# Optimization experiments

Measured on AMD Instinct MI355X. Metric: run time of the kernel, lower is better.

Reference implementation:

```python
import jax, jax.numpy as jnp
import numpy as np

NTOKENS = 50257
NHID = 1024
NPC = int(np.ceil(np.sqrt(NTOKENS)))            # 225 tokens per class
NCLASSES = int(np.ceil(NTOKENS / NPC))          # 224 classes
BATCH = 1024
INITRANGE = 0.1


def setup_inputs() -> dict:
    key = jax.random.key(0)
    k1, k2, k3, k4 = jax.random.split(key, 4)
    inputs = jax.random.normal(k1, (BATCH, NHID), dtype=jnp.float32)
    labels = jax.random.randint(k2, (BATCH,), 0, NTOKENS, dtype=jnp.int64)
    layer_top_W = jax.random.uniform(k3, (NHID, NCLASSES), minval=-INITRANGE, maxval=INITRANGE, dtype=jnp.float32)
    layer_top_b = jnp.zeros((NCLASSES,), dtype=jnp.float32)
    layer_bottom_W = jax.random.uniform(k4, (NCLASSES, NHID, NPC), minval=-INITRANGE, maxval=INITRANGE, dtype=jnp.float32)
    layer_bottom_b = jnp.zeros((NCLASSES, NPC), dtype=jnp.float32)
    return {
        "inputs": inputs,
        "labels": labels,
        "layer_top_W": layer_top_W,
        "layer_top_b": layer_top_b,
        "layer_bottom_W": layer_bottom_W,
        "layer_bottom_b": layer_bottom_b,
    }


def reference(inputs, labels, layer_top_W, layer_top_b, layer_bottom_W, layer_bottom_b):
    batch_size = inputs.shape[0]
    # decompose label into (class, within-class) position; old-torch `/` on Long == floor div
    pos_top = labels // NPC            # [B]
    pos_bottom = labels % NPC          # [B]

    # top-level class distribution: [B, nclasses]
    top_logits = inputs @ layer_top_W + layer_top_b
    top_probs = jax.nn.softmax(top_logits, axis=1)

    # gather per-sample class weight slices and do batched matvec:
    # layer_bottom_W[pos_top]: [B, nhid, npc]
    bottom_logits = jnp.einsum("bd,bdc->bc", inputs, layer_bottom_W[pos_top]) + layer_bottom_b[pos_top]
    bottom_probs = jax.nn.softmax(bottom_logits, axis=1)

    rows = jnp.arange(batch_size)
    target_probs = top_probs[rows, pos_top] * bottom_probs[rows, pos_bottom]  # [B]
    return target_probs
```

## Files before the change

### kernel.cpp

```cpp
#include <hip/hip_runtime.h>
#include <math.h>

#define NHID 1024
#define NPC  225
#define NCLS 224
#define BATCH 1024
#define N_TOP (BATCH / 8)

#define WS_PT 0
#define WS_PB 1024

__global__ __launch_bounds__(1024, 4) void k_fused(const float* __restrict__ X,
                                                   const int* __restrict__ labels,
                                                   const float* __restrict__ Wt,
                                                   const float* __restrict__ bt,
                                                   const float* __restrict__ Wb,
                                                   const float* __restrict__ bb,
                                                   float* __restrict__ ws)
{
    __shared__ __align__(16) float sm[14848];
    __shared__ int slist[128];
    __shared__ int scnt;

    const int tid  = threadIdx.x;
    const int wave = tid >> 6;
    const int lane = tid & 63;
    const int j8   = tid & 7;
    const int t8   = tid >> 3;

    if ((int)blockIdx.x < NCLS) {
        const int cls = blockIdx.x;
        if (tid == 0) scnt = 0;
        __syncthreads();
        {
            const int lab = labels[tid];
            if (lab / NPC == cls) {
                const int p = atomicAdd(&scnt, 1);
                if (p < 128) slist[p] = tid;
            }
        }
        __syncthreads();
        const int cnt = scnt;
        if (cnt == 0) return;

        const int c0 = lane, c1 = lane + 64, c2 = lane + 128, c3 = lane + 192;
        const bool m3 = (c3 < NPC);
        const int d0 = wave * 64;
        const float* Wr = Wb + (size_t)cls * (NHID * NPC) + (size_t)d0 * NPC;

        for (int base = 0; base < cnt; base += 8) {
            const int nt = min(8, cnt - base);

            const int sid = (j8 < nt) ? slist[base + j8] : -1;
            for (int d4 = t8; d4 < 256; d4 += 128) {
                float4 v = make_float4(0.f, 0.f, 0.f, 0.f);
                if (sid >= 0) v = ((const float4*)&X[(size_t)sid * NHID])[d4];
                float* p = &sm[48 * d4 + j8];
                p[0] = v.x; p[12] = v.y; p[24] = v.z; p[36] = v.w;
            }
            __syncthreads();

            float acc[8][4];
#pragma unroll
            for (int j = 0; j < 8; ++j)
#pragma unroll
                for (int k = 0; k < 4; ++k) acc[j][k] = 0.f;

            auto ldrow = [&](int r, float* o) {
                const float* p = Wr + (size_t)r * NPC;
                o[0] = __builtin_nontemporal_load(p + c0);
                o[1] = __builtin_nontemporal_load(p + c1);
                o[2] = __builtin_nontemporal_load(p + c2);
                o[3] = m3 ? __builtin_nontemporal_load(p + c3) : 0.f;
            };
            float wbuf[4][4];
            ldrow(0, wbuf[0]); ldrow(1, wbuf[1]); ldrow(2, wbuf[2]); ldrow(3, wbuf[3]);

#pragma unroll 4
            for (int dd = 0; dd < 64; ++dd) {
                const int slot = dd & 3;
                const float cw0 = wbuf[slot][0], cw1 = wbuf[slot][1],
                            cw2 = wbuf[slot][2], cw3 = wbuf[slot][3];
                ldrow(min(dd + 4, 63), wbuf[slot]);
                const float4 a = *(const float4*)&sm[(d0 + dd) * 12 + 0];
                const float4 b = *(const float4*)&sm[(d0 + dd) * 12 + 4];
                const float xi[8] = {a.x, a.y, a.z, a.w, b.x, b.y, b.z, b.w};
#pragma unroll
                for (int j = 0; j < 8; ++j) {
                    acc[j][0] = fmaf(xi[j], cw0, acc[j][0]);
                    acc[j][1] = fmaf(xi[j], cw1, acc[j][1]);
                    acc[j][2] = fmaf(xi[j], cw2, acc[j][2]);
                    acc[j][3] = fmaf(xi[j], cw3, acc[j][3]);
                }
            }
            __syncthreads();

            float* red = sm;
            if (wave >= 8) {
#pragma unroll
                for (int j = 0; j < 8; ++j)
#pragma unroll
                    for (int k = 0; k < 4; ++k) {
                        int c = lane + 64 * k;
                        if (c < NPC) red[((wave - 8) * 8 + j) * 232 + c] = acc[j][k];
                    }
            }
            __syncthreads();
            if (wave < 8) {
#pragma unroll
                for (int j = 0; j < 8; ++j)
#pragma unroll
                    for (int k = 0; k < 4; ++k) {
                        int c = lane + 64 * k;
                        if (c < NPC) red[(wave * 8 + j) * 232 + c] += acc[j][k];
                    }
            }
            __syncthreads();

            if (wave < 8) {
                const int j = wave;
                if (j < nt) {
                    const int s = slist[base + j];
                    float v[4];
#pragma unroll
                    for (int k = 0; k < 4; ++k) {
                        int c = lane + 64 * k;
                        if (c < NPC) {
                            float t = bb[(size_t)cls * NPC + c];
#pragma unroll
                            for (int g = 0; g < 8; ++g) t += red[(g * 8 + j) * 232 + c];
                            v[k] = t;
                        } else v[k] = -INFINITY;
                    }
                    float m = fmaxf(fmaxf(v[0], v[1]), fmaxf(v[2], v[3]));
                    for (int o = 32; o > 0; o >>= 1) m = fmaxf(m, __shfl_xor(m, o));
                    float e = expf(v[0] - m) + expf(v[1] - m) + expf(v[2] - m) + expf(v[3] - m);
                    for (int o = 32; o > 0; o >>= 1) e += __shfl_xor(e, o);
                    const int pb = labels[s] % NPC;
                    if (lane == (pb & 63))
                        ws[WS_PB + s] = expf(v[pb >> 6] - m) / e;
                }
            }
            __syncthreads();
        }
        return;
    }

    const int sbase = (blockIdx.x - NCLS) * 8;

    for (int d4 = t8; d4 < 256; d4 += 128) {
        const float4 v = ((const float4*)&X[(size_t)(sbase + j8) * NHID])[d4];
        float* p = &sm[48 * d4 + j8];
        p[0] = v.x; p[12] = v.y; p[24] = v.z; p[36] = v.w;
    }
    __syncthreads();

    float acc[8][4];
#pragma unroll
    for (int j = 0; j < 8; ++j)
#pragma unroll
        for (int k = 0; k < 4; ++k) acc[j][k] = 0.f;

    const int c0 = lane, c1 = lane + 64, c2 = lane + 128, c3 = lane + 192;
    const bool m3 = (c3 < NCLS);
    const int d0 = wave * 64;
    const float* Wr = Wt + (size_t)d0 * NCLS;

    auto ldrow = [&](int r, float* o) {
        const float* p = Wr + (size_t)r * NCLS;
        o[0] = p[c0]; o[1] = p[c1]; o[2] = p[c2];
        o[3] = m3 ? p[c3] : 0.f;
    };
    float wbuf[4][4];
    ldrow(0, wbuf[0]); ldrow(1, wbuf[1]); ldrow(2, wbuf[2]); ldrow(3, wbuf[3]);

#pragma unroll 4
    for (int dd = 0; dd < 64; ++dd) {
        const int slot = dd & 3;
        const float cw0 = wbuf[slot][0], cw1 = wbuf[slot][1],
                    cw2 = wbuf[slot][2], cw3 = wbuf[slot][3];
        ldrow(min(dd + 4, 63), wbuf[slot]);
        const float4 a = *(const float4*)&sm[(d0 + dd) * 12 + 0];
        const float4 b = *(const float4*)&sm[(d0 + dd) * 12 + 4];
        const float xi[8] = {a.x, a.y, a.z, a.w, b.x, b.y, b.z, b.w};
#pragma unroll
        for (int j = 0; j < 8; ++j) {
            acc[j][0] = fmaf(xi[j], cw0, acc[j][0]);
            acc[j][1] = fmaf(xi[j], cw1, acc[j][1]);
            acc[j][2] = fmaf(xi[j], cw2, acc[j][2]);
            acc[j][3] = fmaf(xi[j], cw3, acc[j][3]);
        }
    }
    __syncthreads();

    float* red = sm;
    if (wave >= 8) {
#pragma unroll
        for (int j = 0; j < 8; ++j)
#pragma unroll
            for (int k = 0; k < 4; ++k) {
                int c = lane + 64 * k;
                if (c < NCLS) red[((wave - 8) * 8 + j) * 232 + c] = acc[j][k];
            }
    }
    __syncthreads();
    if (wave < 8) {
#pragma unroll
        for (int j = 0; j < 8; ++j)
#pragma unroll
            for (int k = 0; k < 4; ++k) {
                int c = lane + 64 * k;
                if (c < NCLS) red[(wave * 8 + j) * 232 + c] += acc[j][k];
            }
    }
    __syncthreads();

    if (wave < 8) {
        const int j = wave;
        const int s = sbase + j;
        float v[4];
#pragma unroll
        for (int k = 0; k < 4; ++k) {
            int c = lane + 64 * k;
            if (c < NCLS) {
                float t = bt[c];
#pragma unroll
                for (int g = 0; g < 8; ++g) t += red[(g * 8 + j) * 232 + c];
                v[k] = t;
            } else v[k] = -INFINITY;
        }
        float m = fmaxf(fmaxf(v[0], v[1]), fmaxf(v[2], v[3]));
        for (int o = 32; o > 0; o >>= 1) m = fmaxf(m, __shfl_xor(m, o));
        float e = expf(v[0] - m) + expf(v[1] - m) + expf(v[2] - m) + expf(v[3] - m);
        for (int o = 32; o > 0; o >>= 1) e += __shfl_xor(e, o);
        const int pt = labels[s] / NPC;
        if (lane == (pt & 63))
            ws[WS_PT + s] = expf(v[pt >> 6] - m) / e;
    }
}

__global__ void k_mul(const float* __restrict__ ws, float* __restrict__ out)
{
    const int i = blockIdx.x * 256 + threadIdx.x;
    if (i < BATCH) out[i] = ws[WS_PT + i] * ws[WS_PB + i];
}

extern "C" void kernel_launch(void* const* d_in, const int* in_sizes, int n_in,
                              void* d_out, int out_size, void* d_ws, size_t ws_size,
                              hipStream_t stream)
{
    const float* X      = (const float*)d_in[0];
    const int*   labels = (const int*)  d_in[1];
    const float* Wt     = (const float*)d_in[2];
    const float* bt     = (const float*)d_in[3];
    const float* Wb     = (const float*)d_in[4];
    const float* bb     = (const float*)d_in[5];

    hipLaunchKernelGGL(k_fused, dim3(NCLS + N_TOP), dim3(1024), 0, stream,
                       X, labels, Wt, bt, Wb, bb, (float*)d_ws);
    hipLaunchKernelGGL(k_mul, dim3(BATCH / 256), dim3(256), 0, stream,
                       (const float*)d_ws, (float*)d_out);
}
```

Measured before the change: 345.8 us.

## Split bottom-layer work into one block per 8-sample chunk of each class

```diff
diff --git a/kernel.cpp b/kernel.cpp
--- a/kernel.cpp
+++ b/kernel.cpp
@@ -5,6 +5,7 @@
 #define NPC  225
 #define NCLS 224
 #define BATCH 1024
+#define N_BOT 352
 #define N_TOP (BATCH / 8)
 
 #define WS_PT 0
@@ -19,8 +20,11 @@
                                                    float* __restrict__ ws)
 {
     __shared__ __align__(16) float sm[14848];
-    __shared__ int slist[128];
-    __shared__ int scnt;
+    __shared__ int cnt_[256];
+    __shared__ int iscan_[256];
+    __shared__ int slot[8];
+    __shared__ int wtot[16];
+    __shared__ int cls_sh;
 
     const int tid  = threadIdx.x;
     const int wave = tid >> 6;
@@ -28,125 +32,148 @@
     const int j8   = tid & 7;
     const int t8   = tid >> 3;
 
-    if ((int)blockIdx.x < NCLS) {
-        const int cls = blockIdx.x;
-        if (tid == 0) scnt = 0;
-        __syncthreads();
+    if ((int)blockIdx.x < N_BOT) {
+        if (tid < 256) cnt_[tid] = 0;
+        __syncthreads();
+        const int myc = labels[tid] / NPC;
+        atomicAdd(&cnt_[myc], 1);
+        __syncthreads();
+        if (tid < 256) iscan_[tid] = (tid < NCLS) ? ((cnt_[tid] + 7) >> 3) : 0;
+        __syncthreads();
+        for (int off = 1; off < 256; off <<= 1) {
+            int a = 0;
+            if (tid < 256 && tid >= off) a = iscan_[tid - off];
+            __syncthreads();
+            if (tid < 256) iscan_[tid] += a;
+            __syncthreads();
+        }
+        if ((int)blockIdx.x >= iscan_[255]) return;
+        if (tid < NCLS) {
+            const int lo = (tid == 0) ? 0 : iscan_[tid - 1];
+            if ((int)blockIdx.x >= lo && (int)blockIdx.x < iscan_[tid]) cls_sh = tid;
+        }
+        __syncthreads();
+        const int cls    = cls_sh;
+        const int ibase  = (cls == 0) ? 0 : iscan_[cls - 1];
+        const int within = (int)blockIdx.x - ibase;
+        const int cnt    = cnt_[cls];
+        const int nt     = min(8, cnt - 8 * within);
+
         {
-            const int lab = labels[tid];
-            if (lab / NPC == cls) {
-                const int p = atomicAdd(&scnt, 1);
-                if (p < 128) slist[p] = tid;
-            }
-        }
-        __syncthreads();
-        const int cnt = scnt;
-        if (cnt == 0) return;
+            const bool flag = (myc == cls);
+            const unsigned long long m = __ballot(flag);
+            if (lane == 0) wtot[wave] = __popcll(m);
+            __syncthreads();
+            if (flag) {
+                int pos = __popcll(m & ((1ull << lane) - 1));
+#pragma unroll
+                for (int w = 0; w < 16; ++w)
+                    if (w < wave) pos += wtot[w];
+                const int r = pos - 8 * within;
+                if (r >= 0 && r < 8) slot[r] = tid;
+            }
+            __syncthreads();
+        }
+
+        const int sid = (j8 < nt) ? slot[j8] : -1;
+        for (int d4 = t8; d4 < 256; d4 += 128) {
+            float4 v = make_float4(0.f, 0.f, 0.f, 0.f);
+            if (sid >= 0) v = ((const float4*)&X[(size_t)sid * NHID])[d4];
+            float* p = &sm[48 * d4 + j8];
+            p[0] = v.x; p[12] = v.y; p[24] = v.z; p[36] = v.w;
+        }
+        __syncthreads();
+
+        float acc[8][4];
+#pragma unroll
+        for (int j = 0; j < 8; ++j)
+#pragma unroll
+            for (int k = 0; k < 4; ++k) acc[j][k] = 0.f;
 
         const int c0 = lane, c1 = lane + 64, c2 = lane + 128, c3 = lane + 192;
         const bool m3 = (c3 < NPC);
         const int d0 = wave * 64;
         const float* Wr = Wb + (size_t)cls * (NHID * NPC) + (size_t)d0 * NPC;
 
-        for (int base = 0; base < cnt; base += 8) {
-            const int nt = min(8, cnt - base);
-
-            const int sid = (j8 < nt) ? slist[base + j8] : -1;
-            for (int d4 = t8; d4 < 256; d4 += 128) {
-                float4 v = make_float4(0.f, 0.f, 0.f, 0.f);
-                if (sid >= 0) v = ((const float4*)&X[(size_t)sid * NHID])[d4];
-                float* p = &sm[48 * d4 + j8];
-                p[0] = v.x; p[12] = v.y; p[24] = v.z; p[36] = v.w;
-            }
-            __syncthreads();
-
-            float acc[8][4];
+        auto ldrow = [&](int r, float* o) {
+            const float* p = Wr + (size_t)r * NPC;
+            o[0] = __builtin_nontemporal_load(p + c0);
+            o[1] = __builtin_nontemporal_load(p + c1);
+            o[2] = __builtin_nontemporal_load(p + c2);
+            o[3] = m3 ? __builtin_nontemporal_load(p + c3) : 0.f;
+        };
+        float wbuf[4][4];
+        ldrow(0, wbuf[0]); ldrow(1, wbuf[1]); ldrow(2, wbuf[2]); ldrow(3, wbuf[3]);
+
+#pragma unroll 4
+        for (int dd = 0; dd < 64; ++dd) {
+            const int slot4 = dd & 3;
+            const float cw0 = wbuf[slot4][0], cw1 = wbuf[slot4][1],
+                        cw2 = wbuf[slot4][2], cw3 = wbuf[slot4][3];
+            ldrow(min(dd + 4, 63), wbuf[slot4]);
+            const float4 a = *(const float4*)&sm[(d0 + dd) * 12 + 0];
+            const float4 b = *(const float4*)&sm[(d0 + dd) * 12 + 4];
+            const float xi[8] = {a.x, a.y, a.z, a.w, b.x, b.y, b.z, b.w};
+#pragma unroll
+            for (int j = 0; j < 8; ++j) {
+                acc[j][0] = fmaf(xi[j], cw0, acc[j][0]);
+                acc[j][1] = fmaf(xi[j], cw1, acc[j][1]);
+                acc[j][2] = fmaf(xi[j], cw2, acc[j][2]);
+                acc[j][3] = fmaf(xi[j], cw3, acc[j][3]);
+            }
+        }
+        __syncthreads();
+
+        float* red = sm;
+        if (wave >= 8) {
 #pragma unroll
             for (int j = 0; j < 8; ++j)
 #pragma unroll
-                for (int k = 0; k < 4; ++k) acc[j][k] = 0.f;
-
-            auto ldrow = [&](int r, float* o) {
-                const float* p = Wr + (size_t)r * NPC;
-                o[0] = __builtin_nontemporal_load(p + c0);
-                o[1] = __builtin_nontemporal_load(p + c1);
-                o[2] = __builtin_nontemporal_load(p + c2);
-                o[3] = m3 ? __builtin_nontemporal_load(p + c3) : 0.f;
-            };
-            float wbuf[4][4];
-            ldrow(0, wbuf[0]); ldrow(1, wbuf[1]); ldrow(2, wbuf[2]); ldrow(3, wbuf[3]);
-
-#pragma unroll 4
-            for (int dd = 0; dd < 64; ++dd) {
-                const int slot = dd & 3;
-                const float cw0 = wbuf[slot][0], cw1 = wbuf[slot][1],
-                            cw2 = wbuf[slot][2], cw3 = wbuf[slot][3];
-                ldrow(min(dd + 4, 63), wbuf[slot]);
-                const float4 a = *(const float4*)&sm[(d0 + dd) * 12 + 0];
-                const float4 b = *(const float4*)&sm[(d0 + dd) * 12 + 4];
-                const float xi[8] = {a.x, a.y, a.z, a.w, b.x, b.y, b.z, b.w};
-#pragma unroll
-                for (int j = 0; j < 8; ++j) {
-                    acc[j][0] = fmaf(xi[j], cw0, acc[j][0]);
-                    acc[j][1] = fmaf(xi[j], cw1, acc[j][1]);
-                    acc[j][2] = fmaf(xi[j], cw2, acc[j][2]);
-                    acc[j][3] = fmaf(xi[j], cw3, acc[j][3]);
+                for (int k = 0; k < 4; ++k) {
+                    int c = lane + 64 * k;
+                    if (c < NPC) red[((wave - 8) * 8 + j) * 232 + c] = acc[j][k];
                 }
-            }
-            __syncthreads();
-
-            float* red = sm;
-            if (wave >= 8) {
-#pragma unroll
-                for (int j = 0; j < 8; ++j)
-#pragma unroll
-                    for (int k = 0; k < 4; ++k) {
-                        int c = lane + 64 * k;
-                        if (c < NPC) red[((wave - 8) * 8 + j) * 232 + c] = acc[j][k];
-                    }
-            }
-            __syncthreads();
-            if (wave < 8) {
-#pragma unroll
-                for (int j = 0; j < 8; ++j)
-#pragma unroll
-                    for (int k = 0; k < 4; ++k) {
-                        int c = lane + 64 * k;
-                        if (c < NPC) red[(wave * 8 + j) * 232 + c] += acc[j][k];
-                    }
-            }
-            __syncthreads();
-
-            if (wave < 8) {
-                const int j = wave;
-                if (j < nt) {
-                    const int s = slist[base + j];
-                    float v[4];
-#pragma unroll
-                    for (int k = 0; k < 4; ++k) {
-                        int c = lane + 64 * k;
-                        if (c < NPC) {
-                            float t = bb[(size_t)cls * NPC + c];
-#pragma unroll
-                            for (int g = 0; g < 8; ++g) t += red[(g * 8 + j) * 232 + c];
-                            v[k] = t;
-                        } else v[k] = -INFINITY;
-                    }
-                    float m = fmaxf(fmaxf(v[0], v[1]), fmaxf(v[2], v[3]));
-                    for (int o = 32; o > 0; o >>= 1) m = fmaxf(m, __shfl_xor(m, o));
-                    float e = expf(v[0] - m) + expf(v[1] - m) + expf(v[2] - m) + expf(v[3] - m);
-                    for (int o = 32; o > 0; o >>= 1) e += __shfl_xor(e, o);
-                    const int pb = labels[s] % NPC;
-                    if (lane == (pb & 63))
-                        ws[WS_PB + s] = expf(v[pb >> 6] - m) / e;
+        }
+        __syncthreads();
+        if (wave < 8) {
+#pragma unroll
+            for (int j = 0; j < 8; ++j)
+#pragma unroll
+                for (int k = 0; k < 4; ++k) {
+                    int c = lane + 64 * k;
+                    if (c < NPC) red[(wave * 8 + j) * 232 + c] += acc[j][k];
                 }
-            }
-            __syncthreads();
+        }
+        __syncthreads();
+
+        if (wave < 8) {
+            const int j = wave;
+            if (j < nt) {
+                const int s = slot[j];
+                float v[4];
+#pragma unroll
+                for (int k = 0; k < 4; ++k) {
+                    int c = lane + 64 * k;
+                    if (c < NPC) {
+                        float t = bb[(size_t)cls * NPC + c];
+#pragma unroll
+                        for (int g = 0; g < 8; ++g) t += red[(g * 8 + j) * 232 + c];
+                        v[k] = t;
+                    } else v[k] = -INFINITY;
+                }
+                float m = fmaxf(fmaxf(v[0], v[1]), fmaxf(v[2], v[3]));
+                for (int o = 32; o > 0; o >>= 1) m = fmaxf(m, __shfl_xor(m, o));
+                float e = expf(v[0] - m) + expf(v[1] - m) + expf(v[2] - m) + expf(v[3] - m);
+                for (int o = 32; o > 0; o >>= 1) e += __shfl_xor(e, o);
+                const int pb = labels[s] % NPC;
+                if (lane == (pb & 63))
+                    ws[WS_PB + s] = expf(v[pb >> 6] - m) / e;
+            }
         }
         return;
     }
 
-    const int sbase = (blockIdx.x - NCLS) * 8;
+    const int sbase = ((int)blockIdx.x - N_BOT) * 8;
 
     for (int d4 = t8; d4 < 256; d4 += 128) {
         const float4 v = ((const float4*)&X[(size_t)(sbase + j8) * NHID])[d4];
@@ -176,10 +203,10 @@
 
 #pragma unroll 4
     for (int dd = 0; dd < 64; ++dd) {
-        const int slot = dd & 3;
-        const float cw0 = wbuf[slot][0], cw1 = wbuf[slot][1],
-                    cw2 = wbuf[slot][2], cw3 = wbuf[slot][3];
-        ldrow(min(dd + 4, 63), wbuf[slot]);
+        const int slot4 = dd & 3;
+        const float cw0 = wbuf[slot4][0], cw1 = wbuf[slot4][1],
+                    cw2 = wbuf[slot4][2], cw3 = wbuf[slot4][3];
+        ldrow(min(dd + 4, 63), wbuf[slot4]);
         const float4 a = *(const float4*)&sm[(d0 + dd) * 12 + 0];
         const float4 b = *(const float4*)&sm[(d0 + dd) * 12 + 4];
         const float xi[8] = {a.x, a.y, a.z, a.w, b.x, b.y, b.z, b.w};
@@ -256,7 +283,7 @@
     const float* Wb     = (const float*)d_in[4];
     const float* bb     = (const float*)d_in[5];
 
-    hipLaunchKernelGGL(k_fused, dim3(NCLS + N_TOP), dim3(1024), 0, stream,
+    hipLaunchKernelGGL(k_fused, dim3(N_BOT + N_TOP), dim3(1024), 0, stream,
                        X, labels, Wt, bt, Wb, bb, (float*)d_ws);
     hipLaunchKernelGGL(k_mul, dim3(BATCH / 256), dim3(256), 0, stream,
                        (const float*)d_ws, (float*)d_out);
```

New measurement: 304.1 us. 1.14x faster.
